# Kernel tuning notes

Measured on AMD Instinct MI355X. Metric: run time of the kernel, lower is better.

Reference implementation:

```python
import jax, jax.numpy as jnp
import numpy as np

B, C, N, H = 4, 512, 2048, 8
D = C // H  # per-head depth = 64
EPS = 1e-5


def conv1x1(x, W, b):
    # x: [B, Cin, N], W: [Cout, Cin], b: [Cout]
    return jnp.einsum('oc,bcn->bon', W, x) + b[None, :, None]


def instance_norm(x):
    # normalize over length dim per (batch, channel), no affine
    mu = jnp.mean(x, axis=-1, keepdims=True)
    var = jnp.var(x, axis=-1, keepdims=True)
    return (x - mu) * jax.lax.rsqrt(var + EPS)


def _pipeline(src, tgt, Wq, bq, Wk, bk, Wv, bv, Wm, bm):
    # query from src, key/value from tgt; reshape C -> (D outer, H inner)
    q = conv1x1(src, Wq, bq).reshape(B, D, H, N)
    k = conv1x1(tgt, Wk, bk).reshape(B, D, H, N)
    v = conv1x1(tgt, Wv, bv).reshape(B, D, H, N)
    scores = jnp.einsum('bdhn,bdhm->bhnm', q, k) / jnp.sqrt(jnp.float32(D))
    probs = jax.nn.softmax(scores, axis=-1)
    out = jnp.einsum('bhnm,bdhm->bdhn', probs, v).reshape(B, C, N)
    return conv1x1(out, Wm, bm)


def _mlp(x, W1, b1, W2, b2):
    h = conv1x1(x, W1, b1)
    h = jax.nn.relu(instance_norm(h))
    return conv1x1(h, W2, b2)


def setup_inputs() -> dict:
    key = jax.random.key(0)
    ks = jax.random.split(key, 8)
    s = 0.02
    return {
        'source_features': jax.random.normal(ks[0], (B, C, N), jnp.float32),
        'target_features': jax.random.normal(ks[1], (B, C, N), jnp.float32),
        'Wq': jax.random.normal(ks[2], (C, C), jnp.float32) * s,
        'bq': jnp.zeros((C,), jnp.float32),
        'Wk': jax.random.normal(ks[3], (C, C), jnp.float32) * s,
        'bk': jnp.zeros((C,), jnp.float32),
        'Wv': jax.random.normal(ks[4], (C, C), jnp.float32) * s,
        'bv': jnp.zeros((C,), jnp.float32),
        'Wm': jax.random.normal(ks[5], (C, C), jnp.float32) * s,
        'bm': jnp.zeros((C,), jnp.float32),
        'W1': jax.random.normal(ks[6], (2 * C, 2 * C), jnp.float32) * s,
        'b1': jnp.zeros((2 * C,), jnp.float32),
        'W2': jax.random.normal(ks[7], (C, 2 * C), jnp.float32) * s,
        'b2': jnp.zeros((C,), jnp.float32),
    }


def reference(source_features, target_features, Wq, bq, Wk, bk, Wv, bv, Wm, bm, W1, b1, W2, b2):
    src, tgt = source_features, target_features
    # source update uses ORIGINAL target features
    src_att = _pipeline(src, tgt, Wq, bq, Wk, bk, Wv, bv, Wm, bm)
    src = src + _mlp(jnp.concatenate([src, src_att], axis=1), W1, b1, W2, b2)
    # target update uses the UPDATED source features (in-place semantics of original)
    tgt_att = _pipeline(tgt, src, Wq, bq, Wk, bk, Wv, bv, Wm, bm)
    tgt = tgt + _mlp(jnp.concatenate([tgt, tgt_att], axis=1), W1, b1, W2, b2)
    return src, tgt
```

## Files before the change

### kernel.cpp

```cpp
#include <hip/hip_runtime.h>

#define NN 2048
#define CC 512
#define BB 4
#define HH 8
#define DD 64
#define SCALE 0.18033688011112043f

typedef unsigned short u16;
typedef __attribute__((ext_vector_type(8))) short bf16x8;
typedef __attribute__((ext_vector_type(4))) float f32x4;

extern "C" __device__ float __ocml_native_exp2_f32(float);

__device__ inline u16 f2b(float x) {
    unsigned u = __builtin_bit_cast(unsigned, x);
    u += 0x7fffu + ((u >> 16) & 1u);
    return (u16)(u >> 16);
}
__device__ inline float b2f(u16 h) {
    unsigned u = ((unsigned)h) << 16;
    return __builtin_bit_cast(float, u);
}

#define GLD16(g, l) __builtin_amdgcn_global_load_lds( \
    (const __attribute__((address_space(1))) unsigned int*)(g), \
    (__attribute__((address_space(3))) unsigned int*)(l), 16, 0, 0)

template<int JT>
__device__ __forceinline__ void gemm_core_t(
    const u16* __restrict__ Xa, const u16* __restrict__ Xb, int Ca, int K,
    const u16* __restrict__ Wt, size_t rowBase,
    u16* As, u16* Bs, f32x4 (&acc)[4][JT])
{
    constexpr int OT = JT * 32;
    const int tid = threadIdx.x;
    const int lane = tid & 63, w = tid >> 6;
    const int quad = lane >> 4, l16 = lane & 15;
    const int wrow = w & 1, wcol = w >> 1;
    const int arow = lane >> 2, aseg = lane & 3;

    for (int k0 = 0; k0 < K; k0 += 32) {
        const u16* Xs; int Crow, cc;
        if (k0 < Ca) { Xs = Xa; Crow = Ca; cc = k0; }
        else         { Xs = Xb; Crow = K - Ca; cc = k0 - Ca; }
#pragma unroll
        for (int i = 0; i < 2; ++i) {
            int rl = w * 32 + i * 16 + arow;
            int la = __builtin_amdgcn_readfirstlane((w * 32 + i * 16) * 32);
            GLD16(Xs + (rowBase + rl) * (size_t)Crow + cc + aseg * 8, (char*)As + (size_t)la * 2);
        }
#pragma unroll
        for (int i = 0; i < OT / 64; ++i) {
            int rl = w * (OT / 4) + i * 16 + arow;
            int la = __builtin_amdgcn_readfirstlane((w * (OT / 4) + i * 16) * 32);
            GLD16(Wt + (size_t)rl * K + k0 + aseg * 8, (char*)Bs + (size_t)la * 2);
        }
        __syncthreads();
        bf16x8 av[4], bv[JT];
#pragma unroll
        for (int i = 0; i < 4; ++i)
            av[i] = *(const bf16x8*)&As[(wrow * 64 + i * 16 + l16) * 32 + quad * 8];
#pragma unroll
        for (int jj = 0; jj < JT; ++jj)
            bv[jj] = *(const bf16x8*)&Bs[(wcol * JT * 16 + jj * 16 + l16) * 32 + quad * 8];
#pragma unroll
        for (int i = 0; i < 4; ++i)
#pragma unroll
            for (int jj = 0; jj < JT; ++jj)
                acc[i][jj] = __builtin_amdgcn_mfma_f32_16x16x32_bf16(av[i], bv[jj], acc[i][jj], 0, 0, 0);
        __syncthreads();
    }
}

template<int JT>
__device__ __forceinline__ void gemm_epilogue_t(
    f32x4 (&acc)[4][JT], const float* __restrict__ bias, int mode,
    int b, int n0, int o0, int Cout,
    const float* __restrict__ res, float* __restrict__ outF, u16* __restrict__ outB)
{
    const int tid = threadIdx.x;
    const int lane = tid & 63, w = tid >> 6;
    const int quad = lane >> 4, l16 = lane & 15;
    const int wrow = w & 1, wcol = w >> 1;
    const size_t bN = (size_t)b * NN;
    const int nb0 = n0 + wrow * 64, ob0 = o0 + wcol * JT * 16;

    if (mode == 0) {
#pragma unroll
        for (int j = 0; j < JT; ++j) {
            int o = ob0 + j * 16 + l16;
            float bs = bias[o];
#pragma unroll
            for (int i = 0; i < 4; ++i)
#pragma unroll
                for (int r = 0; r < 4; ++r) {
                    int n = nb0 + i * 16 + quad * 4 + r;
                    outB[(bN + n) * Cout + o] = f2b(acc[i][j][r] + bs);
                }
        }
    } else if (mode == 1) {
#pragma unroll
        for (int j = 0; j < JT; ++j) {
            int o = ob0 + j * 16 + l16;
            float bs = bias[o];
            int h = o >> 6, d = o & 63;
#pragma unroll
            for (int i = 0; i < 4; ++i) {
                int n = nb0 + i * 16 + quad * 4;
                ushort4 pk;
                pk.x = f2b(acc[i][j][0] + bs); pk.y = f2b(acc[i][j][1] + bs);
                pk.z = f2b(acc[i][j][2] + bs); pk.w = f2b(acc[i][j][3] + bs);
                *(ushort4*)&outB[(((size_t)b * HH + h) * DD + d) * NN + n] = pk;
            }
        }
    } else {
#pragma unroll
        for (int j = 0; j < JT; ++j) {
            int o = ob0 + j * 16 + l16;
            float bs = bias[o];
#pragma unroll
            for (int i = 0; i < 4; ++i) {
                int n = nb0 + i * 16 + quad * 4;
                size_t ad = ((size_t)b * Cout + o) * NN + n;
                float4 rv = *(const float4*)&res[ad];
                float4 yv;
                yv.x = acc[i][j][0] + bs + rv.x;
                yv.y = acc[i][j][1] + bs + rv.y;
                yv.z = acc[i][j][2] + bs + rv.z;
                yv.w = acc[i][j][3] + bs + rv.w;
                *(float4*)&outF[ad] = yv;
                if (mode == 2) {
                    outB[(bN + n + 0) * Cout + o] = f2b(yv.x);
                    outB[(bN + n + 1) * Cout + o] = f2b(yv.y);
                    outB[(bN + n + 2) * Cout + o] = f2b(yv.z);
                    outB[(bN + n + 3) * Cout + o] = f2b(yv.w);
                }
            }
        }
    }
}

template<int JT>
__global__ __launch_bounds__(256, (JT == 2 ? 4 : 3)) void gemm_bf16_t(
    const u16* __restrict__ Wb, const float* __restrict__ bias,
    const u16* __restrict__ Xa, const u16* __restrict__ Xb,
    int Ca, int K, int Cout,
    const float* __restrict__ res, float* __restrict__ outF,
    u16* __restrict__ outB, int mode)
{
    __shared__ u16 As[128 * 32];
    __shared__ u16 Bs[JT * 32 * 32];
    const int b = blockIdx.z, n0 = blockIdx.x * 128, o0 = blockIdx.y * (JT * 32);
    f32x4 acc[4][JT] = {};
    gemm_core_t<JT>(Xa, Xb, Ca, K, Wb + (size_t)o0 * K, (size_t)b * NN + n0, As, Bs, acc);
    gemm_epilogue_t<JT>(acc, bias, mode, b, n0, o0, Cout, res, outF, outB);
}

__global__ __launch_bounds__(256, 3) void gemm_qkv(
    const u16* __restrict__ WQ, const float* __restrict__ bQ,
    const u16* __restrict__ XQ, u16* __restrict__ outQ,
    const u16* __restrict__ WK, const float* __restrict__ bK, u16* __restrict__ outK,
    const u16* __restrict__ WV, const float* __restrict__ bV, u16* __restrict__ outV,
    const u16* __restrict__ XKV)
{
    __shared__ u16 As[128 * 32];
    __shared__ u16 Bs[128 * 32];
    const int yb = blockIdx.y;
    const u16* W; const float* bias; const u16* X; u16* outB; int mode, o0;
    if (yb < 4)      { o0 = yb * 128;       W = WQ; bias = bQ; X = XQ;  outB = outQ; mode = 0; }
    else if (yb < 8) { o0 = (yb - 4) * 128; W = WK; bias = bK; X = XKV; outB = outK; mode = 0; }
    else             { o0 = (yb - 8) * 128; W = WV; bias = bV; X = XKV; outB = outV; mode = 1; }
    const int b = blockIdx.z, n0 = blockIdx.x * 128;
    f32x4 acc[4][4] = {};
    gemm_core_t<4>(X, nullptr, 512, 512, W + (size_t)o0 * 512, (size_t)b * NN + n0, As, Bs, acc);
    gemm_epilogue_t<4>(acc, bias, mode, b, n0, o0, 512, nullptr, nullptr, outB);
}

__global__ __launch_bounds__(256, 4) void attn(
    const u16* __restrict__ Qg, const u16* __restrict__ Kg,
    const u16* __restrict__ Vg, u16* __restrict__ Og)
{
    __shared__ __align__(16) u16 Ks[2][64 * 64];
    __shared__ __align__(16) u16 Vt[2][64 * 64];
    __shared__ __align__(16) u16 Ps[64 * 64];
    const int tid = threadIdx.x;
    const int lane = tid & 63, w = tid >> 6;
    const int quad = lane >> 4, l16 = lane & 15;
    const int id = blockIdx.x;
    const int xcd = id & 7, jj = id >> 3;
    const int bh = xcd * 4 + (jj >> 5), nb = jj & 31;
    const int b = bh >> 3, h = bh & 7;
    const int n0 = nb * 64, wn0 = w * 16;
    const size_t qkBase = ((size_t)b * NN) * CC + h * DD;
    const size_t vBase  = (((size_t)b * HH + h) * DD) * NN;
    const int r8 = lane >> 3, seg = lane & 7;
    const int segp = seg ^ r8;
    const int lk = l16 & 7;

    const u16* kp0 = Kg + qkBase + (size_t)(wn0 + r8) * CC + segp * 8;
    const u16* kp1 = kp0 + (size_t)8 * CC;
    const u16* vp0 = Vg + vBase + (size_t)(wn0 + r8) * NN + segp * 8;
    const u16* vp1 = vp0 + (size_t)8 * NN;

    bf16x8 qf[2];
    {
        int n = n0 + wn0 + l16;
#pragma unroll
        for (int ks = 0; ks < 2; ++ks)
            qf[ks] = *(const bf16x8*)&Qg[qkBase + (size_t)n * CC + ks * 32 + quad * 8];
    }

    const short oneb = 0x3F80;
    const bf16x8 ones = {oneb, oneb, oneb, oneb, oneb, oneb, oneb, oneb};
    f32x4 oa[4] = {};
    f32x4 lacc = {};

    GLD16(kp0, &Ks[0][wn0 * 64]);
    GLD16(kp1, &Ks[0][(wn0 + 8) * 64]);
    GLD16(vp0, &Vt[0][wn0 * 64]);
    GLD16(vp1, &Vt[0][(wn0 + 8) * 64]);
    kp0 += 64 * CC; kp1 += 64 * CC; vp0 += 64; vp1 += 64;

#define ATTN_PREF(BUF) do { \
        GLD16(kp0, &Ks[BUF][wn0 * 64]); \
        GLD16(kp1, &Ks[BUF][(wn0 + 8) * 64]); \
        GLD16(vp0, &Vt[BUF][wn0 * 64]); \
        GLD16(vp1, &Vt[BUF][(wn0 + 8) * 64]); \
        kp0 += 64 * CC; kp1 += 64 * CC; vp0 += 64; vp1 += 64; \
    } while (0)

#define ATTN_BODY(CUR) do { \
        const u16* ksb = Ks[CUR]; \
        const u16* vtb = Vt[CUR]; \
        f32x4 st[4] = {}; \
        _Pragma("unroll") \
        for (int ks = 0; ks < 2; ++ks) { \
            bf16x8 ak[4]; \
            _Pragma("unroll") \
            for (int rt = 0; rt < 4; ++rt) \
                ak[rt] = *(const bf16x8*)&ksb[(rt * 16 + l16) * 64 + ((ks * 4 + quad) ^ lk) * 8]; \
            __builtin_amdgcn_s_setprio(1); \
            _Pragma("unroll") \
            for (int rt = 0; rt < 4; ++rt) \
                st[rt] = __builtin_amdgcn_mfma_f32_16x16x32_bf16(ak[rt], qf[ks], st[rt], 0, 0, 0); \
            __builtin_amdgcn_s_setprio(0); \
        } \
        { \
            int nrow = wn0 + l16; \
            _Pragma("unroll") \
            for (int rt = 0; rt < 4; ++rt) { \
                unsigned u0 = __builtin_bit_cast(unsigned, __ocml_native_exp2_f32(st[rt][0])); \
                unsigned u1 = __builtin_bit_cast(unsigned, __ocml_native_exp2_f32(st[rt][1])); \
                unsigned u2 = __builtin_bit_cast(unsigned, __ocml_native_exp2_f32(st[rt][2])); \
                unsigned u3 = __builtin_bit_cast(unsigned, __ocml_native_exp2_f32(st[rt][3])); \
                uint2 t; \
                t.x = __builtin_amdgcn_perm(u1, u0, 0x07060302u); \
                t.y = __builtin_amdgcn_perm(u3, u2, 0x07060302u); \
                int g = (rt * 2 + (quad >> 1)) ^ lk; \
                *(uint2*)&Ps[nrow * 64 + g * 8 + (quad & 1) * 4] = t; \
            } \
        } \
        _Pragma("unroll") \
        for (int ks = 0; ks < 2; ++ks) { \
            bf16x8 pa = *(const bf16x8*)&Ps[(wn0 + l16) * 64 + ((ks * 4 + quad) ^ lk) * 8]; \
            bf16x8 vb[4]; \
            _Pragma("unroll") \
            for (int ct = 0; ct < 4; ++ct) \
                vb[ct] = *(const bf16x8*)&vtb[(ct * 16 + l16) * 64 + ((ks * 4 + quad) ^ lk) * 8]; \
            __builtin_amdgcn_s_setprio(1); \
            _Pragma("unroll") \
            for (int ct = 0; ct < 4; ++ct) \
                oa[ct] = __builtin_amdgcn_mfma_f32_16x16x32_bf16(pa, vb[ct], oa[ct], 0, 0, 0); \
            lacc = __builtin_amdgcn_mfma_f32_16x16x32_bf16(pa, ones, lacc, 0, 0, 0); \
            __builtin_amdgcn_s_setprio(0); \
        } \
    } while (0)

    for (int it = 0; it < NN / 64; it += 2) {
        __syncthreads();
        ATTN_PREF(1);
        ATTN_BODY(0);
        __syncthreads();
        if (it < NN / 64 - 2)
            ATTN_PREF(0);
        ATTN_BODY(1);
    }
#undef ATTN_PREF
#undef ATTN_BODY

#pragma unroll
    for (int r = 0; r < 4; ++r) {
        float li = 1.f / lacc[r];
        int n = n0 + wn0 + quad * 4 + r;
#pragma unroll
        for (int ct = 0; ct < 4; ++ct)
            Og[qkBase + (size_t)n * CC + ct * 16 + l16] = f2b(oa[ct][r] * li);
    }
}

__global__ __launch_bounds__(256) void transpose_cvt(
    const float* __restrict__ X, u16* __restrict__ Y)
{
    __shared__ float T[64][65];
    const int tid = threadIdx.x;
    const int n0 = blockIdx.x * 64, c0 = blockIdx.y * 64, b = blockIdx.z;
    const int rr = tid >> 4, cc4 = tid & 15;
#pragma unroll
    for (int p = 0; p < 4; ++p) {
        int cl = p * 16 + rr;
        float4 v = *(const float4*)&X[((size_t)b * CC + c0 + cl) * NN + n0 + cc4 * 4];
        T[cl][cc4 * 4 + 0] = v.x; T[cl][cc4 * 4 + 1] = v.y;
        T[cl][cc4 * 4 + 2] = v.z; T[cl][cc4 * 4 + 3] = v.w;
    }
    __syncthreads();
#pragma unroll
    for (int p = 0; p < 4; ++p) {
        int nl = p * 16 + rr;
        ushort4 pk;
        pk.x = f2b(T[cc4 * 4 + 0][nl]);
        pk.y = f2b(T[cc4 * 4 + 1][nl]);
        pk.z = f2b(T[cc4 * 4 + 2][nl]);
        pk.w = f2b(T[cc4 * 4 + 3][nl]);
        *(ushort4*)&Y[((size_t)b * NN + n0 + nl) * CC + c0 + cc4 * 4] = pk;
    }
}

__global__ __launch_bounds__(256) void prep_weights(
    const float* __restrict__ Wq, const float* __restrict__ Wk,
    const float* __restrict__ Wv, const float* __restrict__ Wm,
    const float* __restrict__ W1, const float* __restrict__ W2,
    u16* oQ, u16* oK, u16* oV, u16* oM, u16* o1, u16* o2)
{
    const float* W; u16* o; int rows, cols, perm; float sc = 1.f;
    switch (blockIdx.z) {
        case 0: W = Wq; o = oQ; rows = 512;  cols = 512;  perm = 1; sc = SCALE; break;
        case 1: W = Wk; o = oK; rows = 512;  cols = 512;  perm = 1; break;
        case 2: W = Wv; o = oV; rows = 512;  cols = 512;  perm = 1; break;
        case 3: W = Wm; o = oM; rows = 512;  cols = 512;  perm = 2; break;
        case 4: W = W1; o = o1; rows = 1024; cols = 1024; perm = 0; break;
        default: W = W2; o = o2; rows = 512; cols = 1024; perm = 0; break;
    }
    int c = blockIdx.x * 256 + threadIdx.x;
    int r = blockIdx.y;
    if (r >= rows || c >= cols) return;
    int sr = r, scol = c;
    if (perm == 1) sr = (r & 63) * 8 + (r >> 6);
    else if (perm == 2) scol = (c & 63) * 8 + (c >> 6);
    o[(size_t)r * cols + c] = f2b(W[(size_t)sr * cols + scol] * sc);
}

__global__ void prep_bias(const float* __restrict__ bq, const float* __restrict__ bk,
                          const float* __restrict__ bv,
                          float* oq, float* ok, float* ov)
{
    int i = blockIdx.x * 256 + threadIdx.x;
    int y = blockIdx.y;
    const float* s = (y == 0) ? bq : (y == 1) ? bk : bv;
    float* o = (y == 0) ? oq : (y == 1) ? ok : ov;
    float v = s[(i & 63) * 8 + (i >> 6)];
    if (y == 0) v *= SCALE;
    o[i] = v;
}

__global__ __launch_bounds__(256) void inorm_p1(
    const u16* __restrict__ X, float* __restrict__ Ssum, float* __restrict__ Ssq)
{
    __shared__ float rs[4][64], rq[4][64];
    const int tid = threadIdx.x;
    const int cl = tid & 63, g = tid >> 6;
    const int c = blockIdx.x * 64 + cl;
    const int b = blockIdx.y, nz = blockIdx.z;
    float s = 0.f, q = 0.f;
    size_t base = ((size_t)b * NN + nz * 256 + g * 64) * 1024 + c;
#pragma unroll 4
    for (int i = 0; i < 64; ++i) {
        float x = b2f(X[base + (size_t)i * 1024]);
        s += x; q += x * x;
    }
    rs[g][cl] = s; rq[g][cl] = q;
    __syncthreads();
    if (g == 0) {
        s = rs[0][cl] + rs[1][cl] + rs[2][cl] + rs[3][cl];
        q = rq[0][cl] + rq[1][cl] + rq[2][cl] + rq[3][cl];
        atomicAdd(&Ssum[b * 1024 + c], s);
        atomicAdd(&Ssq[b * 1024 + c], q);
    }
}

__global__ __launch_bounds__(256) void inorm_p2(
    u16* __restrict__ X, const float* __restrict__ Ssum, const float* __restrict__ Ssq)
{
    const int tid = threadIdx.x;
    const int cl = tid & 63, g = tid >> 6;
    const int c = blockIdx.x * 64 + cl;
    const int b = blockIdx.y, nz = blockIdx.z;
    float mean = Ssum[b * 1024 + c] * (1.f / NN);
    float var  = Ssq[b * 1024 + c] * (1.f / NN) - mean * mean;
    float rstd = rsqrtf(fmaxf(var, 0.f) + 1e-5f);
    size_t base = ((size_t)b * NN + nz * 256 + g * 64) * 1024 + c;
#pragma unroll 4
    for (int i = 0; i < 64; ++i) {
        float x = b2f(X[base + (size_t)i * 1024]);
        x = (x - mean) * rstd;
        X[base + (size_t)i * 1024] = f2b(fmaxf(x, 0.f));
    }
}

extern "C" void kernel_launch(void* const* d_in, const int* in_sizes, int n_in,
                              void* d_out, int out_size, void* d_ws, size_t ws_size,
                              hipStream_t stream)
{
    (void)in_sizes; (void)n_in; (void)out_size; (void)ws_size;
    const float* src = (const float*)d_in[0];
    const float* tgt = (const float*)d_in[1];
    const float* Wq = (const float*)d_in[2];  const float* bq = (const float*)d_in[3];
    const float* Wk = (const float*)d_in[4];  const float* bk = (const float*)d_in[5];
    const float* Wv = (const float*)d_in[6];  const float* bv = (const float*)d_in[7];
    const float* Wm = (const float*)d_in[8];  const float* bm = (const float*)d_in[9];
    const float* W1 = (const float*)d_in[10]; const float* b1 = (const float*)d_in[11];
    const float* W2 = (const float*)d_in[12]; const float* b2 = (const float*)d_in[13];

    char* w = (char*)d_ws;
    u16* WQp = (u16*)(w);
    u16* WKp = (u16*)(w + (512u << 10));
    u16* WVp = (u16*)(w + (1u << 20));
    u16* WMp = (u16*)(w + (3u << 19));
    u16* W1b = (u16*)(w + (2u << 20));
    u16* W2b = (u16*)(w + (4u << 20));
    float* BQp = (float*)(w + (5u << 20));
    float* BKp = BQp + 512;
    float* BVp = BQp + 1024;
    float* STS = BQp + 1536;
    float* STQ = STS + 4096;
    u16* X0 = (u16*)(w + ( 6u << 20));
    u16* X1 = (u16*)(w + (14u << 20));
    u16* B0 = (u16*)(w + (22u << 20));
    u16* B1 = (u16*)(w + (30u << 20));
    u16* B2 = (u16*)(w + (38u << 20));
    u16* B3 = (u16*)(w + (46u << 20));

    float* out = (float*)d_out;
    const size_t R = (size_t)BB * CC * NN;
    dim3 blk(256);

    prep_weights<<<dim3(4, 1024, 6), blk, 0, stream>>>(Wq, Wk, Wv, Wm, W1, W2,
                                                       WQp, WKp, WVp, WMp, W1b, W2b);
    prep_bias<<<dim3(2, 3), blk, 0, stream>>>(bq, bk, bv, BQp, BKp, BVp);
    transpose_cvt<<<dim3(32, 8, 4), blk, 0, stream>>>(src, X0);
    transpose_cvt<<<dim3(32, 8, 4), blk, 0, stream>>>(tgt, X1);

    dim3 gQKV(16, 12, 4), gM(16, 8, 4), gW1(16, 8, 4), gW2(16, 8, 4);

    gemm_qkv<<<gQKV, blk, 0, stream>>>(WQp, BQp, X0, B0, WKp, BKp, B1, WVp, BVp, B2, X1);
    attn<<<dim3(1024), blk, 0, stream>>>(B0, B1, B2, B3);
    gemm_bf16_t<2><<<gM, blk, 0, stream>>>(WMp, bm, B3, nullptr, 512, 512, 512, nullptr, nullptr, B0, 0);
    gemm_bf16_t<4><<<gW1, blk, 0, stream>>>(W1b, b1, X0, B0, 512, 1024, 1024, nullptr, nullptr, B1, 0);
    hipMemsetAsync(STS, 0, 8192 * sizeof(float), stream);
    inorm_p1<<<dim3(16, 4, 8), blk, 0, stream>>>(B1, STS, STQ);
    inorm_p2<<<dim3(16, 4, 8), blk, 0, stream>>>(B1, STS, STQ);
    gemm_bf16_t<2><<<gW2, blk, 0, stream>>>(W2b, b2, B1, nullptr, 1024, 1024, 512, src, out, B3, 2);

    gemm_qkv<<<gQKV, blk, 0, stream>>>(WQp, BQp, X1, X0, WKp, BKp, B0, WVp, BVp, B1, B3);
    attn<<<dim3(1024), blk, 0, stream>>>(X0, B0, B1, B2);
    gemm_bf16_t<2><<<gM, blk, 0, stream>>>(WMp, bm, B2, nullptr, 512, 512, 512, nullptr, nullptr, X0, 0);
    gemm_bf16_t<4><<<gW1, blk, 0, stream>>>(W1b, b1, X1, X0, 512, 1024, 1024, nullptr, nullptr, B0, 0);
    hipMemsetAsync(STS, 0, 8192 * sizeof(float), stream);
    inorm_p1<<<dim3(16, 4, 8), blk, 0, stream>>>(B0, STS, STQ);
    inorm_p2<<<dim3(16, 4, 8), blk, 0, stream>>>(B0, STS, STQ);
    gemm_bf16_t<2><<<gW2, blk, 0, stream>>>(W2b, b2, B0, nullptr, 1024, 1024, 512, tgt, out + R, nullptr, 3);
}
```

Baseline: 424.6 us.

## Double attention query tile per block to reuse K/V loads

Each attention block now handles 128 query rows instead of 64, with each wave owning two 16-row query sub-tiles that share the same K and V fragments read from shared memory. This halves the grid, halving global K/V traffic and LDS fragment reads per query. In exchange it uses more registers (launch bounds drop from 4 to 2 blocks per CU), a larger P buffer, and gives 512 blocks, which reduces the parallelism available to hide latency.

```diff
diff --git a/kernel.cpp b/kernel.cpp
--- a/kernel.cpp
+++ b/kernel.cpp
@@ -177,63 +177,65 @@
     gemm_epilogue_t<4>(acc, bias, mode, b, n0, o0, 512, nullptr, nullptr, outB);
 }
 
-__global__ __launch_bounds__(256, 4) void attn(
+__global__ __launch_bounds__(256, 2) void attn(
     const u16* __restrict__ Qg, const u16* __restrict__ Kg,
     const u16* __restrict__ Vg, u16* __restrict__ Og)
 {
     __shared__ __align__(16) u16 Ks[2][64 * 64];
     __shared__ __align__(16) u16 Vt[2][64 * 64];
-    __shared__ __align__(16) u16 Ps[64 * 64];
+    __shared__ __align__(16) u16 Ps[128 * 64];
     const int tid = threadIdx.x;
     const int lane = tid & 63, w = tid >> 6;
     const int quad = lane >> 4, l16 = lane & 15;
     const int id = blockIdx.x;
     const int xcd = id & 7, jj = id >> 3;
-    const int bh = xcd * 4 + (jj >> 5), nb = jj & 31;
+    const int bh = xcd * 4 + (jj >> 4), nb = jj & 15;
     const int b = bh >> 3, h = bh & 7;
-    const int n0 = nb * 64, wn0 = w * 16;
+    const int n0 = nb * 128, wn0 = w * 32;
+    const int sr0 = w * 16;
     const size_t qkBase = ((size_t)b * NN) * CC + h * DD;
     const size_t vBase  = (((size_t)b * HH + h) * DD) * NN;
     const int r8 = lane >> 3, seg = lane & 7;
     const int segp = seg ^ r8;
     const int lk = l16 & 7;
 
-    const u16* kp0 = Kg + qkBase + (size_t)(wn0 + r8) * CC + segp * 8;
+    const u16* kp0 = Kg + qkBase + (size_t)(sr0 + r8) * CC + segp * 8;
     const u16* kp1 = kp0 + (size_t)8 * CC;
-    const u16* vp0 = Vg + vBase + (size_t)(wn0 + r8) * NN + segp * 8;
+    const u16* vp0 = Vg + vBase + (size_t)(sr0 + r8) * NN + segp * 8;
     const u16* vp1 = vp0 + (size_t)8 * NN;
 
-    bf16x8 qf[2];
-    {
-        int n = n0 + wn0 + l16;
+    bf16x8 qf[2][2];
+#pragma unroll
+    for (int qs = 0; qs < 2; ++qs) {
+        int n = n0 + wn0 + qs * 16 + l16;
 #pragma unroll
         for (int ks = 0; ks < 2; ++ks)
-            qf[ks] = *(const bf16x8*)&Qg[qkBase + (size_t)n * CC + ks * 32 + quad * 8];
+            qf[qs][ks] = *(const bf16x8*)&Qg[qkBase + (size_t)n * CC + ks * 32 + quad * 8];
     }
 
     const short oneb = 0x3F80;
     const bf16x8 ones = {oneb, oneb, oneb, oneb, oneb, oneb, oneb, oneb};
-    f32x4 oa[4] = {};
-    f32x4 lacc = {};
-
-    GLD16(kp0, &Ks[0][wn0 * 64]);
-    GLD16(kp1, &Ks[0][(wn0 + 8) * 64]);
-    GLD16(vp0, &Vt[0][wn0 * 64]);
-    GLD16(vp1, &Vt[0][(wn0 + 8) * 64]);
+    f32x4 oa[2][4] = {};
+    f32x4 lacc[2] = {};
+
+    GLD16(kp0, &Ks[0][sr0 * 64]);
+    GLD16(kp1, &Ks[0][(sr0 + 8) * 64]);
+    GLD16(vp0, &Vt[0][sr0 * 64]);
+    GLD16(vp1, &Vt[0][(sr0 + 8) * 64]);
     kp0 += 64 * CC; kp1 += 64 * CC; vp0 += 64; vp1 += 64;
 
 #define ATTN_PREF(BUF) do { \
-        GLD16(kp0, &Ks[BUF][wn0 * 64]); \
-        GLD16(kp1, &Ks[BUF][(wn0 + 8) * 64]); \
-        GLD16(vp0, &Vt[BUF][wn0 * 64]); \
-        GLD16(vp1, &Vt[BUF][(wn0 + 8) * 64]); \
+        GLD16(kp0, &Ks[BUF][sr0 * 64]); \
+        GLD16(kp1, &Ks[BUF][(sr0 + 8) * 64]); \
+        GLD16(vp0, &Vt[BUF][sr0 * 64]); \
+        GLD16(vp1, &Vt[BUF][(sr0 + 8) * 64]); \
         kp0 += 64 * CC; kp1 += 64 * CC; vp0 += 64; vp1 += 64; \
     } while (0)
 
 #define ATTN_BODY(CUR) do { \
         const u16* ksb = Ks[CUR]; \
         const u16* vtb = Vt[CUR]; \
-        f32x4 st[4] = {}; \
+        f32x4 st[2][4] = {}; \
         _Pragma("unroll") \
         for (int ks = 0; ks < 2; ++ks) { \
             bf16x8 ak[4]; \
@@ -243,17 +245,20 @@
             __builtin_amdgcn_s_setprio(1); \
             _Pragma("unroll") \
             for (int rt = 0; rt < 4; ++rt) \
-                st[rt] = __builtin_amdgcn_mfma_f32_16x16x32_bf16(ak[rt], qf[ks], st[rt], 0, 0, 0); \
+                _Pragma("unroll") \
+                for (int qs = 0; qs < 2; ++qs) \
+                    st[qs][rt] = __builtin_amdgcn_mfma_f32_16x16x32_bf16(ak[rt], qf[qs][ks], st[qs][rt], 0, 0, 0); \
             __builtin_amdgcn_s_setprio(0); \
         } \
-        { \
-            int nrow = wn0 + l16; \
+        _Pragma("unroll") \
+        for (int qs = 0; qs < 2; ++qs) { \
+            int nrow = wn0 + qs * 16 + l16; \
             _Pragma("unroll") \
             for (int rt = 0; rt < 4; ++rt) { \
-                unsigned u0 = __builtin_bit_cast(unsigned, __ocml_native_exp2_f32(st[rt][0])); \
-                unsigned u1 = __builtin_bit_cast(unsigned, __ocml_native_exp2_f32(st[rt][1])); \
-                unsigned u2 = __builtin_bit_cast(unsigned, __ocml_native_exp2_f32(st[rt][2])); \
-                unsigned u3 = __builtin_bit_cast(unsigned, __ocml_native_exp2_f32(st[rt][3])); \
+                unsigned u0 = __builtin_bit_cast(unsigned, __ocml_native_exp2_f32(st[qs][rt][0])); \
+                unsigned u1 = __builtin_bit_cast(unsigned, __ocml_native_exp2_f32(st[qs][rt][1])); \
+                unsigned u2 = __builtin_bit_cast(unsigned, __ocml_native_exp2_f32(st[qs][rt][2])); \
+                unsigned u3 = __builtin_bit_cast(unsigned, __ocml_native_exp2_f32(st[qs][rt][3])); \
                 uint2 t; \
                 t.x = __builtin_amdgcn_perm(u1, u0, 0x07060302u); \
                 t.y = __builtin_amdgcn_perm(u3, u2, 0x07060302u); \
@@ -263,7 +268,10 @@
         } \
         _Pragma("unroll") \
         for (int ks = 0; ks < 2; ++ks) { \
-            bf16x8 pa = *(const bf16x8*)&Ps[(wn0 + l16) * 64 + ((ks * 4 + quad) ^ lk) * 8]; \
+            bf16x8 pa[2]; \
+            _Pragma("unroll") \
+            for (int qs = 0; qs < 2; ++qs) \
+                pa[qs] = *(const bf16x8*)&Ps[(wn0 + qs * 16 + l16) * 64 + ((ks * 4 + quad) ^ lk) * 8]; \
             bf16x8 vb[4]; \
             _Pragma("unroll") \
             for (int ct = 0; ct < 4; ++ct) \
@@ -271,8 +279,12 @@
             __builtin_amdgcn_s_setprio(1); \
             _Pragma("unroll") \
             for (int ct = 0; ct < 4; ++ct) \
-                oa[ct] = __builtin_amdgcn_mfma_f32_16x16x32_bf16(pa, vb[ct], oa[ct], 0, 0, 0); \
-            lacc = __builtin_amdgcn_mfma_f32_16x16x32_bf16(pa, ones, lacc, 0, 0, 0); \
+                _Pragma("unroll") \
+                for (int qs = 0; qs < 2; ++qs) \
+                    oa[qs][ct] = __builtin_amdgcn_mfma_f32_16x16x32_bf16(pa[qs], vb[ct], oa[qs][ct], 0, 0, 0); \
+            _Pragma("unroll") \
+            for (int qs = 0; qs < 2; ++qs) \
+                lacc[qs] = __builtin_amdgcn_mfma_f32_16x16x32_bf16(pa[qs], ones, lacc[qs], 0, 0, 0); \
             __builtin_amdgcn_s_setprio(0); \
         } \
     } while (0)
@@ -290,13 +302,15 @@
 #undef ATTN_BODY
 
 #pragma unroll
-    for (int r = 0; r < 4; ++r) {
-        float li = 1.f / lacc[r];
-        int n = n0 + wn0 + quad * 4 + r;
-#pragma unroll
-        for (int ct = 0; ct < 4; ++ct)
-            Og[qkBase + (size_t)n * CC + ct * 16 + l16] = f2b(oa[ct][r] * li);
-    }
+    for (int qs = 0; qs < 2; ++qs)
+#pragma unroll
+        for (int r = 0; r < 4; ++r) {
+            float li = 1.f / lacc[qs][r];
+            int n = n0 + wn0 + qs * 16 + quad * 4 + r;
+#pragma unroll
+            for (int ct = 0; ct < 4; ++ct)
+                Og[qkBase + (size_t)n * CC + ct * 16 + l16] = f2b(oa[qs][ct][r] * li);
+        }
 }
 
 __global__ __launch_bounds__(256) void transpose_cvt(
@@ -453,7 +467,7 @@
     dim3 gQKV(16, 12, 4), gM(16, 8, 4), gW1(16, 8, 4), gW2(16, 8, 4);
 
     gemm_qkv<<<gQKV, blk, 0, stream>>>(WQp, BQp, X0, B0, WKp, BKp, B1, WVp, BVp, B2, X1);
-    attn<<<dim3(1024), blk, 0, stream>>>(B0, B1, B2, B3);
+    attn<<<dim3(512), blk, 0, stream>>>(B0, B1, B2, B3);
     gemm_bf16_t<2><<<gM, blk, 0, stream>>>(WMp, bm, B3, nullptr, 512, 512, 512, nullptr, nullptr, B0, 0);
     gemm_bf16_t<4><<<gW1, blk, 0, stream>>>(W1b, b1, X0, B0, 512, 1024, 1024, nullptr, nullptr, B1, 0);
     hipMemsetAsync(STS, 0, 8192 * sizeof(float), stream);
@@ -462,7 +476,7 @@
     gemm_bf16_t<2><<<gW2, blk, 0, stream>>>(W2b, b2, B1, nullptr, 1024, 1024, 512, src, out, B3, 2);
 
     gemm_qkv<<<gQKV, blk, 0, stream>>>(WQp, BQp, X1, X0, WKp, BKp, B0, WVp, BVp, B1, B3);
-    attn<<<dim3(1024), blk, 0, stream>>>(X0, B0, B1, B2);
+    attn<<<dim3(512), blk, 0, stream>>>(X0, B0, B1, B2);
     gemm_bf16_t<2><<<gM, blk, 0, stream>>>(WMp, bm, B2, nullptr, 512, 512, 512, nullptr, nullptr, X0, 0);
     gemm_bf16_t<4><<<gW1, blk, 0, stream>>>(W1b, b1, X1, X0, 512, 1024, 1024, nullptr, nullptr, B0, 0);
     hipMemsetAsync(STS, 0, 8192 * sizeof(float), stream);
```

Measured after the change: 417.2 us. About the same (-1.7%).
